# Optimization experiments

Hardware: AMD Instinct MI355X
Metric: run time of the kernel (lower is better)

Reference implementation:

```python
import jax, jax.numpy as jnp
import numpy as np

M_POS = 0.5
M_NEG_SIM = 0.1
LAM_NEG = 1.0


def setup_inputs() -> dict:
    key = jax.random.key(0)
    N, d, G = 8192, 1024, 64
    codebook = jax.random.normal(key, (N, d), dtype=jnp.float32)
    base = (jnp.arange(N) // G) * G  # contiguous groups of size G (vq_to_range)
    starts = base.astype(jnp.int32)
    ends = (base + G - 1).astype(jnp.int32)
    return {"codebook": codebook, "starts": starts, "ends": ends, "max_i": N - 1}


def reference(codebook, starts, ends, max_i):
    N, d = codebook.shape
    M = min(N, int(max_i) + 1)  # rows processed by the python loop

    # cosine similarity rows [0:M] vs all N
    zn = codebook / jnp.linalg.norm(codebook, axis=-1, keepdims=True)
    cos = jnp.einsum('md,nd->mn', zn[:M], zn)  # (M, N)

    # pairwise Euclidean distances rows [0:M] vs all N via ||a-b||^2 = |a|^2+|b|^2-2ab
    sq = jnp.sum(codebook * codebook, axis=-1)  # (N,)
    dot = jnp.einsum('md,nd->mn', codebook[:M], codebook)  # (M, N)
    d2 = jnp.maximum(sq[:M, None] + sq[None, :] - 2.0 * dot, 0.0)

    j = jnp.arange(N)[None, :]
    i = jnp.arange(M)[:, None]
    in_range = (j >= starts[:M, None]) & (j <= ends[:M, None])
    pos_mask = in_range & (j != i)
    # original: group_mask[i]=False then neg = ~group_mask, so i is in negatives
    neg_mask = (~in_range) | (j == i)

    pos_cnt = jnp.sum(pos_mask, axis=-1)
    neg_cnt = jnp.sum(neg_mask, axis=-1)

    # safe sqrt: only evaluate on positive-mask entries
    D = jnp.sqrt(jnp.where(pos_mask, d2, 1.0))
    pos_term = jnp.square(jax.nn.relu(D - M_POS)) * pos_mask
    pos_pull = jnp.sum(pos_term, axis=-1) / jnp.maximum(pos_cnt, 1)

    neg_cos = jnp.clip(cos, -1.0, 1.0)
    neg_term = jnp.square(jax.nn.relu(jnp.abs(neg_cos) - M_NEG_SIM)) * neg_mask
    ortho = jnp.sum(neg_term, axis=-1) / jnp.maximum(neg_cnt, 1)

    valid = (pos_cnt > 0) & (neg_cnt > 0)
    per_row = jnp.where(valid, pos_pull + LAM_NEG * ortho, 0.0)
    cnt = jnp.sum(valid)
    total = jnp.sum(per_row)
    return jnp.where(cnt > 0, total / jnp.maximum(cnt, 1).astype(total.dtype), jnp.zeros((), total.dtype))
```

## Files before the change

### kernel.cpp

```cpp
#include <hip/hip_runtime.h>
#include <hip/hip_bf16.h>
#include <stdint.h>

#define M_POS 0.5f
#define M_NEG 0.1f
#define LAM_NEG 1.0f

typedef __attribute__((ext_vector_type(8))) short short8;
typedef __attribute__((ext_vector_type(4))) float floatx4;

__global__ __launch_bounds__(256) void prep_kernel(
    const float* __restrict__ cb, __hip_bfloat16* __restrict__ cb_bf,
    float* __restrict__ sq, float* __restrict__ inv_norm,
    unsigned* __restrict__ zero_base, int zero_len,
    int N, int d)
{
    const int gi = blockIdx.x * 256 + threadIdx.x;
    if (gi < zero_len) zero_base[gi] = 0u;

    const int wave = threadIdx.x >> 6;
    const int lane = threadIdx.x & 63;
    const int row = blockIdx.x * 4 + wave;
    if (row >= N) return;
    const float* src = cb + (size_t)row * d;
    __hip_bfloat16* dst = cb_bf + (size_t)row * d;

    float s = 0.f;
    for (int c = lane * 4; c < d; c += 256) {
        float4 v = *(const float4*)(src + c);
        s += v.x * v.x + v.y * v.y + v.z * v.z + v.w * v.w;
        __hip_bfloat16 h[4];
        h[0] = __float2bfloat16(v.x);
        h[1] = __float2bfloat16(v.y);
        h[2] = __float2bfloat16(v.z);
        h[3] = __float2bfloat16(v.w);
        *(uint2*)(dst + c) = *(uint2*)h;
    }
    for (int o = 32; o > 0; o >>= 1) s += __shfl_down(s, o, 64);
    if (lane == 0) {
        sq[row] = s;
        inv_norm[row] = rsqrtf(s);
    }
}

__global__ __launch_bounds__(256) void gram_loss_kernel(
    const __hip_bfloat16* __restrict__ A,
    const float* __restrict__ sq, const float* __restrict__ inv_norm,
    const int* __restrict__ starts, const int* __restrict__ ends,
    const int* __restrict__ max_ip,
    float* __restrict__ pos_acc, float* __restrict__ neg_acc,
    int N, int d)
{
    const int M = min(N, max_ip[0] + 1);

    const int t = blockIdx.x;
    int bx = (int)((sqrtf(8.f * (float)t + 1.f) - 1.f) * 0.5f);
    while ((bx + 1) * (bx + 2) / 2 <= t) bx++;
    while (bx * (bx + 1) / 2 > t) bx--;
    const int by = t - bx * (bx + 1) / 2;

    const int rowBase = by * 128;
    const int colBase = bx * 128;
    const bool isDiag = (by == bx);

    __shared__ __hip_bfloat16 ldsA[128 * 64];
    __shared__ __hip_bfloat16 ldsB[128 * 64];

    const int tid  = threadIdx.x;
    const int wave = tid >> 6;
    const int lane = tid & 63;
    const int wr = (wave >> 1) * 64;
    const int wc = (wave & 1) * 64;

    floatx4 acc[4][4];
#pragma unroll
    for (int a = 0; a < 4; ++a)
#pragma unroll
        for (int b = 0; b < 4; ++b) acc[a][b] = (floatx4){0.f, 0.f, 0.f, 0.f};

    const int ldRow = lane >> 3;
    const int dstCol = (lane & 7) * 8;
    const int srcCol = ((lane ^ ldRow) & 7) * 8;
    const int kTiles = d / 64;

    for (int kt = 0; kt < kTiles; ++kt) {
        __syncthreads();
        const int k0 = kt * 64;
#pragma unroll
        for (int q = 0; q < 4; ++q) {
            const int r = q * 32 + wave * 8 + ldRow;
            const __hip_bfloat16* ga = A + (size_t)(rowBase + r) * d + k0 + srcCol;
            const __hip_bfloat16* gb = A + (size_t)(colBase + r) * d + k0 + srcCol;
            __builtin_amdgcn_global_load_lds(
                (const __attribute__((address_space(1))) void*)ga,
                (__attribute__((address_space(3))) void*)(ldsA + r * 64 + dstCol), 16, 0, 0);
            __builtin_amdgcn_global_load_lds(
                (const __attribute__((address_space(1))) void*)gb,
                (__attribute__((address_space(3))) void*)(ldsB + r * 64 + dstCol), 16, 0, 0);
        }
        __syncthreads();

        const int rl = lane & 15;
        const int g  = lane >> 4;
#pragma unroll
        for (int ko = 0; ko < 2; ++ko) {
            const int kc = ko * 4 + g;
            short8 af[4], bf[4];
#pragma unroll
            for (int t4 = 0; t4 < 4; ++t4) {
                const int ra = wr + t4 * 16 + rl;
                const int rb = wc + t4 * 16 + rl;
                af[t4] = *(const short8*)(ldsA + ra * 64 + ((kc ^ (rl & 7)) * 8));
                bf[t4] = *(const short8*)(ldsB + rb * 64 + ((kc ^ (rl & 7)) * 8));
            }
#pragma unroll
            for (int rt = 0; rt < 4; ++rt)
#pragma unroll
                for (int ct = 0; ct < 4; ++ct)
                    acc[rt][ct] = __builtin_amdgcn_mfma_f32_16x16x32_bf16(
                        af[rt], bf[ct], acc[rt][ct], 0, 0, 0);
        }
    }

    const int rl = lane & 15;
    const int q  = lane >> 4;
    const int jlo = colBase + wc;
    const int ilo = rowBase + wr;

    int   jn[4];
    float jinv[4];
    bool  jvalid[4];
#pragma unroll
    for (int ct = 0; ct < 4; ++ct) {
        const int j = jlo + ct * 16 + rl;
        jn[ct]  = j;
        jinv[ct] = inv_norm[j];
        jvalid[ct] = (j < M);
    }

    bool posLane = false;
    {
        const int ri = ilo + lane;
        if (ri < M) posLane |= (ends[ri] >= jlo) && (starts[ri] <= jlo + 63);
        if (!isDiag) {
            const int cj = jlo + lane;
            if (cj < M) posLane |= (ends[cj] >= ilo) && (starts[cj] <= ilo + 63);
        }
    }
    const bool fullPath = (__ballot(posLane) != 0ULL);

    float posc[4] = {0.f, 0.f, 0.f, 0.f};
    float negc[4] = {0.f, 0.f, 0.f, 0.f};

    if (fullPath) {
        int   jns[4], jne[4];
        float jsq[4];
#pragma unroll
        for (int ct = 0; ct < 4; ++ct) {
            jsq[ct] = sq[jn[ct]];
            jns[ct] = jvalid[ct] ? starts[jn[ct]] : 0;
            jne[ct] = jvalid[ct] ? ends[jn[ct]]   : -1;
        }
#pragma unroll
        for (int rt = 0; rt < 4; ++rt) {
            const int ibase = rowBase + wr + rt * 16 + q * 4;
#pragma unroll
            for (int reg = 0; reg < 4; ++reg) {
                const int i = ibase + reg;
                const bool rowValid = (i < M);
                const int ns = rowValid ? starts[i] : 0;
                const int ne = rowValid ? ends[i]   : -1;
                const float iinv = inv_norm[i];
                const float isq  = sq[i];
                float posp = 0.f, negp = 0.f;
#pragma unroll
                for (int ct = 0; ct < 4; ++ct) {
                    const float dot = acc[rt][ct][reg];
                    const int j = jn[ct];
                    float cosv = dot * iinv * jinv[ct];
                    cosv = fminf(fmaxf(cosv, -1.f), 1.f);
                    float tn = fmaxf(fabsf(cosv) - M_NEG, 0.f);
                    const float nterm = tn * tn;
                    const float d2 = fmaxf(isq + jsq[ct] - 2.f * dot, 0.f);
                    float tp = fmaxf(sqrtf(d2) - M_POS, 0.f);
                    const float pterm = tp * tp;
                    const bool dg = (j == i);
                    if (rowValid) {
                        const bool in_r = (j >= ns) && (j <= ne);
                        if (in_r && !dg) posp += pterm;
                        if (!in_r || dg) negp += nterm;
                    }
                    if (!isDiag && jvalid[ct]) {
                        const bool in_c = (i >= jns[ct]) && (i <= jne[ct]);
                        if (in_c && !dg) posc[ct] += pterm;
                        if (!in_c || dg) negc[ct] += nterm;
                    }
                }
#pragma unroll
                for (int m = 1; m < 16; m <<= 1) {
                    posp += __shfl_xor(posp, m, 64);
                    negp += __shfl_xor(negp, m, 64);
                }
                if (rowValid && rl == 0) {
                    atomicAdd(&pos_acc[i], posp);
                    atomicAdd(&neg_acc[i], negp);
                }
            }
        }
        if (!isDiag) {
#pragma unroll
            for (int ct = 0; ct < 4; ++ct) {
                posc[ct] += __shfl_xor(posc[ct], 16, 64);
                posc[ct] += __shfl_xor(posc[ct], 32, 64);
                negc[ct] += __shfl_xor(negc[ct], 16, 64);
                negc[ct] += __shfl_xor(negc[ct], 32, 64);
            }
            if (q == 0) {
#pragma unroll
                for (int ct = 0; ct < 4; ++ct) {
                    if (jvalid[ct]) {
                        atomicAdd(&pos_acc[jn[ct]], posc[ct]);
                        atomicAdd(&neg_acc[jn[ct]], negc[ct]);
                    }
                }
            }
        }
    } else {
#pragma unroll
        for (int rt = 0; rt < 4; ++rt) {
            const int ibase = rowBase + wr + rt * 16 + q * 4;
#pragma unroll
            for (int reg = 0; reg < 4; ++reg) {
                const int i = ibase + reg;
                const float iinv = inv_norm[i];
                float negp = 0.f;
#pragma unroll
                for (int ct = 0; ct < 4; ++ct) {
                    const float dot = acc[rt][ct][reg];
                    float cosv = dot * iinv * jinv[ct];
                    cosv = fminf(fmaxf(cosv, -1.f), 1.f);
                    float tn = fmaxf(fabsf(cosv) - M_NEG, 0.f);
                    const float nterm = tn * tn;
                    negp += nterm;
                    negc[ct] += nterm;
                }
#pragma unroll
                for (int m = 1; m < 16; m <<= 1)
                    negp += __shfl_xor(negp, m, 64);
                if ((i < M) && rl == 0)
                    atomicAdd(&neg_acc[i], negp);
            }
        }
        if (!isDiag) {
#pragma unroll
            for (int ct = 0; ct < 4; ++ct) {
                negc[ct] += __shfl_xor(negc[ct], 16, 64);
                negc[ct] += __shfl_xor(negc[ct], 32, 64);
            }
            if (q == 0) {
#pragma unroll
                for (int ct = 0; ct < 4; ++ct)
                    if (jvalid[ct])
                        atomicAdd(&neg_acc[jn[ct]], negc[ct]);
            }
        }
    }
}

__global__ __launch_bounds__(1024) void finalize_kernel(
    const float* __restrict__ pos_acc, const float* __restrict__ neg_acc,
    const int* __restrict__ starts, const int* __restrict__ ends,
    const int* __restrict__ max_ip, int N, float* __restrict__ out)
{
    const int M = min(N, max_ip[0] + 1);
    const int t = threadIdx.x;
    float total = 0.f;
    int cnt = 0;
    for (int i = t; i < M; i += blockDim.x) {
        const int ns = starts[i], ne = ends[i];
        const int lo = max(ns, 0), hi = min(ne, N - 1);
        const int inr = max(hi - lo + 1, 0);
        const bool dg = (i >= ns) && (i <= ne);
        const int pos_cnt = inr - (dg ? 1 : 0);
        const int neg_cnt = N - inr + (dg ? 1 : 0);
        if (pos_cnt > 0 && neg_cnt > 0) {
            total += pos_acc[i] / (float)max(pos_cnt, 1)
                   + LAM_NEG * neg_acc[i] / (float)max(neg_cnt, 1);
            cnt++;
        }
    }
    for (int o = 32; o > 0; o >>= 1) {
        total += __shfl_down(total, o, 64);
        cnt   += __shfl_down(cnt, o, 64);
    }
    __shared__ float ts[16];
    __shared__ int   cs[16];
    const int w = t >> 6;
    if ((t & 63) == 0) { ts[w] = total; cs[w] = cnt; }
    __syncthreads();
    if (t == 0) {
        float T = 0.f; int C = 0;
        const int nw = blockDim.x >> 6;
        for (int i = 0; i < nw; ++i) { T += ts[i]; C += cs[i]; }
        out[0] = (C > 0) ? T / (float)C : 0.f;
    }
}

extern "C" void kernel_launch(void* const* d_in, const int* in_sizes, int n_in,
                              void* d_out, int out_size, void* d_ws, size_t ws_size,
                              hipStream_t stream) {
    const float* cb     = (const float*)d_in[0];
    const int*   starts = (const int*)d_in[1];
    const int*   ends   = (const int*)d_in[2];
    const int*   max_ip = (const int*)d_in[3];
    float* out = (float*)d_out;

    const int N = in_sizes[1];
    const int d = in_sizes[0] / N;

    char* ws = (char*)d_ws;
    __hip_bfloat16* cb_bf = (__hip_bfloat16*)ws;
    size_t off = ((size_t)N * d * sizeof(__hip_bfloat16) + 255) & ~(size_t)255;
    float* sq       = (float*)(ws + off); off += (size_t)N * 4;
    float* inv_norm = (float*)(ws + off); off += (size_t)N * 4;
    float* pos_acc  = (float*)(ws + off); off += (size_t)N * 4;
    float* neg_acc  = (float*)(ws + off); off += (size_t)N * 4;

    prep_kernel<<<(N + 3) / 4, 256, 0, stream>>>(cb, cb_bf, sq, inv_norm,
                                                 (unsigned*)pos_acc, 2 * N, N, d);

    const int nb = N / 128;
    const int nBlocks = nb * (nb + 1) / 2;
    gram_loss_kernel<<<nBlocks, 256, 0, stream>>>(cb_bf, sq, inv_norm, starts, ends,
                                                  max_ip, pos_acc, neg_acc, N, d);

    finalize_kernel<<<1, 1024, 0, stream>>>(pos_acc, neg_acc, starts, ends, max_ip, N, out);
}
```

Measured before the change: 224.3 us.

## Quantize codebook to FP8 and use FP8 MFMA for Gram matrix

```diff
diff --git a/kernel.cpp b/kernel.cpp
--- a/kernel.cpp
+++ b/kernel.cpp
@@ -6,11 +6,11 @@
 #define M_NEG 0.1f
 #define LAM_NEG 1.0f
 
-typedef __attribute__((ext_vector_type(8))) short short8;
 typedef __attribute__((ext_vector_type(4))) float floatx4;
+using f8x8 = long;
 
 __global__ __launch_bounds__(256) void prep_kernel(
-    const float* __restrict__ cb, __hip_bfloat16* __restrict__ cb_bf,
+    const float* __restrict__ cb, unsigned char* __restrict__ cb_q,
     float* __restrict__ sq, float* __restrict__ inv_norm,
     unsigned* __restrict__ zero_base, int zero_len,
     int N, int d)
@@ -18,33 +18,32 @@
     const int gi = blockIdx.x * 256 + threadIdx.x;
     if (gi < zero_len) zero_base[gi] = 0u;
 
-    const int wave = threadIdx.x >> 6;
-    const int lane = threadIdx.x & 63;
-    const int row = blockIdx.x * 4 + wave;
-    if (row >= N) return;
+    const int row = blockIdx.x;
     const float* src = cb + (size_t)row * d;
-    __hip_bfloat16* dst = cb_bf + (size_t)row * d;
+    unsigned char* dst = cb_q + (size_t)row * d;
+    const int t = threadIdx.x;
 
     float s = 0.f;
-    for (int c = lane * 4; c < d; c += 256) {
+    for (int c = t * 4; c < d; c += 1024) {
         float4 v = *(const float4*)(src + c);
         s += v.x * v.x + v.y * v.y + v.z * v.z + v.w * v.w;
-        __hip_bfloat16 h[4];
-        h[0] = __float2bfloat16(v.x);
-        h[1] = __float2bfloat16(v.y);
-        h[2] = __float2bfloat16(v.z);
-        h[3] = __float2bfloat16(v.w);
-        *(uint2*)(dst + c) = *(uint2*)h;
+        int pk = __builtin_amdgcn_cvt_pk_fp8_f32(v.x, v.y, 0, false);
+        pk     = __builtin_amdgcn_cvt_pk_fp8_f32(v.z, v.w, pk, true);
+        *(int*)(dst + c) = pk;
     }
     for (int o = 32; o > 0; o >>= 1) s += __shfl_down(s, o, 64);
-    if (lane == 0) {
-        sq[row] = s;
-        inv_norm[row] = rsqrtf(s);
+    __shared__ float wsum[4];
+    if ((t & 63) == 0) wsum[t >> 6] = s;
+    __syncthreads();
+    if (t == 0) {
+        float tot = wsum[0] + wsum[1] + wsum[2] + wsum[3];
+        sq[row] = tot;
+        inv_norm[row] = rsqrtf(tot);
     }
 }
 
 __global__ __launch_bounds__(256) void gram_loss_kernel(
-    const __hip_bfloat16* __restrict__ A,
+    const unsigned char* __restrict__ A,
     const float* __restrict__ sq, const float* __restrict__ inv_norm,
     const int* __restrict__ starts, const int* __restrict__ ends,
     const int* __restrict__ max_ip,
@@ -63,8 +62,8 @@
     const int colBase = bx * 128;
     const bool isDiag = (by == bx);
 
-    __shared__ __hip_bfloat16 ldsA[128 * 64];
-    __shared__ __hip_bfloat16 ldsB[128 * 64];
+    __shared__ alignas(16) unsigned char ldsA[128 * 64];
+    __shared__ alignas(16) unsigned char ldsB[128 * 64];
 
     const int tid  = threadIdx.x;
     const int wave = tid >> 6;
@@ -78,51 +77,55 @@
 #pragma unroll
         for (int b = 0; b < 4; ++b) acc[a][b] = (floatx4){0.f, 0.f, 0.f, 0.f};
 
-    const int ldRow = lane >> 3;
-    const int dstCol = (lane & 7) * 8;
-    const int srcCol = ((lane ^ ldRow) & 7) * 8;
+    const int sR = lane >> 2;
+    const int sQ = lane & 3;
     const int kTiles = d / 64;
+
+    const int rl = lane & 15;
+    const int g  = lane >> 4;
+    const int rowx = (rl >> 1) & 3;
+    const int ghalf = g >> 1;
+    const int godd  = (g & 1) * 8;
 
     for (int kt = 0; kt < kTiles; ++kt) {
         __syncthreads();
         const int k0 = kt * 64;
 #pragma unroll
-        for (int q = 0; q < 4; ++q) {
-            const int r = q * 32 + wave * 8 + ldRow;
-            const __hip_bfloat16* ga = A + (size_t)(rowBase + r) * d + k0 + srcCol;
-            const __hip_bfloat16* gb = A + (size_t)(colBase + r) * d + k0 + srcCol;
+        for (int h = 0; h < 2; ++h) {
+            const int r = wave * 32 + h * 16 + sR;
+            const int srcQ = sQ ^ ((r >> 1) & 3);
+            const unsigned char* ga = A + (size_t)(rowBase + r) * d + k0 + srcQ * 16;
+            const unsigned char* gb = A + (size_t)(colBase + r) * d + k0 + srcQ * 16;
             __builtin_amdgcn_global_load_lds(
                 (const __attribute__((address_space(1))) void*)ga,
-                (__attribute__((address_space(3))) void*)(ldsA + r * 64 + dstCol), 16, 0, 0);
+                (__attribute__((address_space(3))) void*)(ldsA + r * 64 + sQ * 16), 16, 0, 0);
             __builtin_amdgcn_global_load_lds(
                 (const __attribute__((address_space(1))) void*)gb,
-                (__attribute__((address_space(3))) void*)(ldsB + r * 64 + dstCol), 16, 0, 0);
+                (__attribute__((address_space(3))) void*)(ldsB + r * 64 + sQ * 16), 16, 0, 0);
         }
         __syncthreads();
 
-        const int rl = lane & 15;
-        const int g  = lane >> 4;
 #pragma unroll
         for (int ko = 0; ko < 2; ++ko) {
-            const int kc = ko * 4 + g;
-            short8 af[4], bf[4];
+            const int phys16 = ((ko * 2 + ghalf) ^ rowx);
+            const int koff = phys16 * 16 + godd;
+            f8x8 af[4], bf[4];
 #pragma unroll
             for (int t4 = 0; t4 < 4; ++t4) {
                 const int ra = wr + t4 * 16 + rl;
                 const int rb = wc + t4 * 16 + rl;
-                af[t4] = *(const short8*)(ldsA + ra * 64 + ((kc ^ (rl & 7)) * 8));
-                bf[t4] = *(const short8*)(ldsB + rb * 64 + ((kc ^ (rl & 7)) * 8));
+                af[t4] = *(const f8x8*)(ldsA + ra * 64 + koff);
+                bf[t4] = *(const f8x8*)(ldsB + rb * 64 + koff);
             }
 #pragma unroll
             for (int rt = 0; rt < 4; ++rt)
 #pragma unroll
                 for (int ct = 0; ct < 4; ++ct)
-                    acc[rt][ct] = __builtin_amdgcn_mfma_f32_16x16x32_bf16(
+                    acc[rt][ct] = __builtin_amdgcn_mfma_f32_16x16x32_fp8_fp8(
                         af[rt], bf[ct], acc[rt][ct], 0, 0, 0);
         }
     }
 
-    const int rl = lane & 15;
     const int q  = lane >> 4;
     const int jlo = colBase + wc;
     const int ilo = rowBase + wr;
@@ -319,19 +322,19 @@
     const int d = in_sizes[0] / N;
 
     char* ws = (char*)d_ws;
-    __hip_bfloat16* cb_bf = (__hip_bfloat16*)ws;
-    size_t off = ((size_t)N * d * sizeof(__hip_bfloat16) + 255) & ~(size_t)255;
+    unsigned char* cb_q = (unsigned char*)ws;
+    size_t off = ((size_t)N * d + 255) & ~(size_t)255;
     float* sq       = (float*)(ws + off); off += (size_t)N * 4;
     float* inv_norm = (float*)(ws + off); off += (size_t)N * 4;
     float* pos_acc  = (float*)(ws + off); off += (size_t)N * 4;
     float* neg_acc  = (float*)(ws + off); off += (size_t)N * 4;
 
-    prep_kernel<<<(N + 3) / 4, 256, 0, stream>>>(cb, cb_bf, sq, inv_norm,
-                                                 (unsigned*)pos_acc, 2 * N, N, d);
+    prep_kernel<<<N, 256, 0, stream>>>(cb, cb_q, sq, inv_norm,
+                                       (unsigned*)pos_acc, 2 * N, N, d);
 
     const int nb = N / 128;
     const int nBlocks = nb * (nb + 1) / 2;
-    gram_loss_kernel<<<nBlocks, 256, 0, stream>>>(cb_bf, sq, inv_norm, starts, ends,
+    gram_loss_kernel<<<nBlocks, 256, 0, stream>>>(cb_q, sq, inv_norm, starts, ends,
                                                   max_ip, pos_acc, neg_acc, N, d);
 
     finalize_kernel<<<1, 1024, 0, stream>>>(pos_acc, neg_acc, starts, ends, max_ip, N, out);
```

Measured after the change: 213.3 us. 1.05x faster.
